# Performance work log

Measured on AMD Instinct MI355X. Metric: run time of the kernel, lower is better.

Reference implementation:

```python
import jax, jax.numpy as jnp
import numpy as np

HEADS = 16
DIM = 1024
D_K = DIM // HEADS
SEQ = 2048


def setup_inputs() -> dict:
    key = jax.random.key(0)
    ks = jax.random.split(key, 11)
    s = 1.0 / np.sqrt(DIM).astype(np.float32)
    return {
        "q": jax.random.normal(ks[0], (SEQ, DIM), jnp.float32),
        "k": jax.random.normal(ks[1], (SEQ, DIM), jnp.float32),
        "v": jax.random.normal(ks[2], (SEQ, DIM), jnp.float32),
        "Wq": jax.random.normal(ks[3], (DIM, DIM), jnp.float32) * s,
        "bq": jax.random.normal(ks[4], (DIM,), jnp.float32) * 0.01,
        "Wk": jax.random.normal(ks[5], (DIM, DIM), jnp.float32) * s,
        "bk": jax.random.normal(ks[6], (DIM,), jnp.float32) * 0.01,
        "Wv": jax.random.normal(ks[7], (DIM, DIM), jnp.float32) * s,
        "bv": jax.random.normal(ks[8], (DIM,), jnp.float32) * 0.01,
        "Wo": jax.random.normal(ks[9], (DIM, DIM), jnp.float32) * s,
        "bo": jax.random.normal(ks[10], (DIM,), jnp.float32) * 0.01,
    }


def reference(q, k, v, Wq, bq, Wk, bk, Wv, bv, Wo, bo):
    S = q.shape[0]
    # torch Linear: x @ W.T + b; view to (1, S, H, d_k) then transpose to (1, H, S, d_k)
    def proj(x, W, b):
        return (x @ W.T + b).reshape(1, S, HEADS, D_K).transpose(0, 2, 1, 3)

    qh = proj(q, Wq, bq)  # (1, H, S, d)
    kh = proj(k, Wk, bk)
    vh = proj(v, Wv, bv)

    scale = 1.0 / np.sqrt(D_K).astype(np.float32)
    scores = jnp.einsum("bhqd,bhkd->bhqk", qh, kh) * scale  # (1, H, S, S)
    # NOTE: source applies softmax over dim=1 == the HEADS axis (faithful quirk)
    attn = jax.nn.softmax(scores, axis=1)
    ctx = jnp.einsum("bhqk,bhkd->bhqd", attn, vh)  # (1, H, S, d)
    concat = ctx.transpose(0, 2, 1, 3).reshape(1, S, DIM)
    return concat @ Wo.T + bo
```

## Files before the change

kernel.cpp:

```cpp
#include <hip/hip_runtime.h>
#include <hip/hip_fp16.h>


typedef _Float16 f16;
typedef _Float16 f16x4 __attribute__((ext_vector_type(4)));
typedef _Float16 f16x8 __attribute__((ext_vector_type(8)));
typedef float    f32x4 __attribute__((ext_vector_type(4)));

#define S_LEN 2048
#define DIM   1024
#define NH    16
#define DK    64
#define EXP2K 0.1803368801111244f

#define MFMA(a, b, c) __builtin_amdgcn_mfma_f32_16x16x32_f16(a, b, c, 0, 0, 0)

#define VM_WAIT0   asm volatile("s_waitcnt vmcnt(0)" ::: "memory")
#define WG_BARRIER asm volatile("s_barrier" ::: "memory")

typedef __attribute__((address_space(1))) void g_void;
typedef __attribute__((address_space(3))) void l_void;

static __device__ __forceinline__ void gload_lds16(const void* g, void* l) {
  __builtin_amdgcn_global_load_lds((g_void*)g, (l_void*)l, 16, 0, 0);
}

static __device__ __forceinline__ float exp_s(float s) {
  return __builtin_amdgcn_exp2f(s * EXP2K);
}

__global__ __launch_bounds__(256) void cvt_all(
    const float* __restrict__ q, const float* __restrict__ k, const float* __restrict__ v,
    const float* __restrict__ Wq, const float* __restrict__ Wk, const float* __restrict__ Wv,
    const float* __restrict__ Wo, f16* __restrict__ qh, f16* __restrict__ kh,
    f16* __restrict__ vh, f16* __restrict__ wqh, f16* __restrict__ wkh,
    f16* __restrict__ wvh, f16* __restrict__ woh) {
  const size_t M = 1048576;
  const int seg = blockIdx.y;
  const float* src;
  f16* dst;
  switch (seg) {
    case 0: src = q;      dst = qh;      break;
    case 1: src = q + M;  dst = qh + M;  break;
    case 2: src = k;      dst = kh;      break;
    case 3: src = k + M;  dst = kh + M;  break;
    case 4: src = v;      dst = vh;      break;
    case 5: src = v + M;  dst = vh + M;  break;
    case 6: src = Wq;     dst = wqh;     break;
    case 7: src = Wk;     dst = wkh;     break;
    case 8: src = Wv;     dst = wvh;     break;
    default: src = Wo;    dst = woh;     break;
  }
  int i = blockIdx.x * 256 + threadIdx.x;
  float4 vv = ((const float4*)src)[i];
  f16x4 o = {(f16)vv.x, (f16)vv.y, (f16)vv.z, (f16)vv.w};
  ((f16x4*)dst)[i] = o;
}

__global__ __launch_bounds__(256) void cvt_f32_f16(const float* __restrict__ src,
                                                   f16* __restrict__ dst, int n4) {
  int i = blockIdx.x * 256 + threadIdx.x;
  if (i < n4) {
    float4 v = ((const float4*)src)[i];
    f16x4 o = {(f16)v.x, (f16)v.y, (f16)v.z, (f16)v.w};
    ((f16x4*)dst)[i] = o;
  }
}

static __device__ __forceinline__ void gemm32_core(const f16* __restrict__ X,
                                                   const f16* __restrict__ W,
                                                   int k0, int k1, int bm, int bn,
                                                   f16* As, f16* Bs,
                                                   f32x4 (&acc)[4][2]) {
  const int tid = threadIdx.x;
  const int wv = tid >> 6;
  const int lane = tid & 63;
  const int qd = lane >> 4;
  const int l16 = lane & 15;
  const int wm = (wv & 1) * 64;
  const int wn = (wv >> 1) * 32;
  const int lr4 = lane >> 2, lc4 = lane & 3;

  const f16* gA = X + (size_t)(bm + wv * 32 + lr4) * DIM + k0 + lc4 * 8;
  const f16* gB = W + (size_t)(bn + wv * 16 + lr4) * DIM + k0 + lc4 * 8;
  const int np = (k1 - k0) >> 5;

  gload_lds16(gA, As + (wv * 32) * 32);
  gload_lds16(gA + 16 * DIM, As + (wv * 32 + 16) * 32);
  gload_lds16(gB, Bs + (wv * 16) * 32);

#pragma unroll 2
  for (int t = 0; t < np; t++) {
    const int buf = t & 1;
    VM_WAIT0;
    WG_BARRIER;
    if (t + 1 < np) {
      const f16* gA1 = gA + (t + 1) * 32;
      const f16* gB1 = gB + (t + 1) * 32;
      f16* dA = As + (buf ^ 1) * (128 * 32);
      f16* dB = Bs + (buf ^ 1) * (64 * 32);
      gload_lds16(gA1, dA + (wv * 32) * 32);
      gload_lds16(gA1 + 16 * DIM, dA + (wv * 32 + 16) * 32);
      gload_lds16(gB1, dB + (wv * 16) * 32);
    }
    const f16* A = As + buf * (128 * 32);
    const f16* B = Bs + buf * (64 * 32);
    f16x8 bf[2];
#pragma unroll
    for (int ni = 0; ni < 2; ni++)
      bf[ni] = *(const f16x8*)&B[(wn + ni * 16 + l16) * 32 + qd * 8];
#pragma unroll
    for (int mi = 0; mi < 4; mi++) {
      f16x8 af = *(const f16x8*)&A[(wm + mi * 16 + l16) * 32 + qd * 8];
#pragma unroll
      for (int ni = 0; ni < 2; ni++)
        acc[mi][ni] = MFMA(af, bf[ni], acc[mi][ni]);
    }
  }
}

__global__ __launch_bounds__(256) void gemm_qkv(
    const f16* __restrict__ X0, const f16* __restrict__ X1, const f16* __restrict__ X2,
    const f16* __restrict__ W0, const f16* __restrict__ W1, const f16* __restrict__ W2,
    const float* __restrict__ b0, const float* __restrict__ b1, const float* __restrict__ b2,
    f16* __restrict__ o0, f16* __restrict__ o1, f16* __restrict__ o2) {
  __shared__ __align__(16) f16 As[2 * 128 * 32];
  __shared__ __align__(16) f16 Bs[2 * 64 * 32];
  const int z = blockIdx.z;
  const f16* X = z == 0 ? X0 : z == 1 ? X1 : X2;
  const f16* W = z == 0 ? W0 : z == 1 ? W1 : W2;
  const float* bias = z == 0 ? b0 : z == 1 ? b1 : b2;
  f16* outh = z == 0 ? o0 : z == 1 ? o1 : o2;

  const int bm = blockIdx.y * 128, bn = blockIdx.x * 64;
  f32x4 acc[4][2];
#pragma unroll
  for (int a = 0; a < 4; a++)
#pragma unroll
    for (int b = 0; b < 2; b++) acc[a][b] = (f32x4){0.f, 0.f, 0.f, 0.f};

  gemm32_core(X, W, 0, DIM, bm, bn, As, Bs, acc);

  const int tid = threadIdx.x;
  const int wv = tid >> 6, lane = tid & 63;
  const int qd = lane >> 4, l16 = lane & 15;
  const int wm = (wv & 1) * 64, wn = (wv >> 1) * 32;
#pragma unroll
  for (int mi = 0; mi < 4; mi++) {
#pragma unroll
    for (int ni = 0; ni < 2; ni++) {
      const int gm = bm + wm + mi * 16 + qd * 4;
      const int gn = bn + wn + ni * 16 + l16;
      const float bs = bias[gn];
      if (z == 2) {
        f16x4 o = {(f16)(acc[mi][ni][0] + bs), (f16)(acc[mi][ni][1] + bs),
                   (f16)(acc[mi][ni][2] + bs), (f16)(acc[mi][ni][3] + bs)};
        *(f16x4*)&outh[(size_t)gn * S_LEN + gm] = o;
      } else {
#pragma unroll
        for (int r = 0; r < 4; r++)
          outh[(size_t)(gm + r) * DIM + gn] = (f16)(acc[mi][ni][r] + bs);
      }
    }
  }
}

__global__ __launch_bounds__(256) void gemm_out(const f16* __restrict__ X,
                                                const f16* __restrict__ W,
                                                const float* __restrict__ bias,
                                                float* __restrict__ outf) {
  __shared__ __align__(16) f16 As[2 * 128 * 32];
  __shared__ __align__(16) f16 Bs[2 * 64 * 32];
  const int z = blockIdx.z;
  const int bm = blockIdx.y * 128, bn = blockIdx.x * 64;
  f32x4 acc[4][2];
#pragma unroll
  for (int a = 0; a < 4; a++)
#pragma unroll
    for (int b = 0; b < 2; b++) acc[a][b] = (f32x4){0.f, 0.f, 0.f, 0.f};

  gemm32_core(X, W, z * (DIM / 2), (z + 1) * (DIM / 2), bm, bn, As, Bs, acc);

  const int tid = threadIdx.x;
  const int wv = tid >> 6, lane = tid & 63;
  const int qd = lane >> 4, l16 = lane & 15;
  const int wm = (wv & 1) * 64, wn = (wv >> 1) * 32;
#pragma unroll
  for (int mi = 0; mi < 4; mi++) {
#pragma unroll
    for (int ni = 0; ni < 2; ni++) {
      const int gm = bm + wm + mi * 16 + qd * 4;
      const int gn = bn + wn + ni * 16 + l16;
      const float bs = z == 0 ? bias[gn] : 0.f;
#pragma unroll
      for (int r = 0; r < 4; r++)
        atomicAdd(&outf[(size_t)(gm + r) * DIM + gn], acc[mi][ni][r] + bs);
    }
  }
}

__global__ __launch_bounds__(256) void attn_denom(const f16* __restrict__ Qp,
                                                  const f16* __restrict__ Kp,
                                                  f16* __restrict__ IDn) {
  __shared__ __align__(16) f16 Qs[2][2][64 * 32];
  __shared__ __align__(16) f16 Ks[2][2][64 * 32];
  const int tid = threadIdx.x;
  const int wv = tid >> 6;
  const int lane = tid & 63;
  const int qd = lane >> 4;
  const int l16 = lane & 15;
  const int wm = (wv & 1) * 32, wn = (wv >> 1) * 32;
  const int bi = blockIdx.y * 64, bj = blockIdx.x * 64;
  const int lr4 = lane >> 2, lc4 = lane & 3;
  const int kkw = wv & 1;
  const int q0 = (wv >> 1) * 2;

  f32x4 dsum[2][2];
#pragma unroll
  for (int a = 0; a < 2; a++)
#pragma unroll
    for (int b = 0; b < 2; b++) dsum[a][b] = (f32x4){0.f, 0.f, 0.f, 0.f};

  {
    const f16* gq = Qp + (size_t)(bi + q0 * 16 + lr4) * DIM + kkw * 32 + lc4 * 8;
    const f16* gk = Kp + (size_t)(bj + q0 * 16 + lr4) * DIM + kkw * 32 + lc4 * 8;
#pragma unroll
    for (int t = 0; t < 2; t++) {
      gload_lds16(gq + (size_t)t * 16 * DIM, &Qs[0][kkw][(q0 + t) * 16 * 32]);
      gload_lds16(gk + (size_t)t * 16 * DIM, &Ks[0][kkw][(q0 + t) * 16 * 32]);
    }
  }

#pragma unroll 2
  for (int h = 0; h < NH; h++) {
    const int buf = h & 1;
    VM_WAIT0;
    WG_BARRIER;
    if (h + 1 < NH) {
      const f16* gq = Qp + (size_t)(bi + q0 * 16 + lr4) * DIM + (h + 1) * DK + kkw * 32 + lc4 * 8;
      const f16* gk = Kp + (size_t)(bj + q0 * 16 + lr4) * DIM + (h + 1) * DK + kkw * 32 + lc4 * 8;
#pragma unroll
      for (int t = 0; t < 2; t++) {
        gload_lds16(gq + (size_t)t * 16 * DIM, &Qs[buf ^ 1][kkw][(q0 + t) * 16 * 32]);
        gload_lds16(gk + (size_t)t * 16 * DIM, &Ks[buf ^ 1][kkw][(q0 + t) * 16 * 32]);
      }
    }

#pragma unroll
    for (int mi = 0; mi < 2; mi++) {
      f16x8 af0 = *(const f16x8*)&Qs[buf][0][(wm + mi * 16 + l16) * 32 + qd * 8];
      f16x8 af1 = *(const f16x8*)&Qs[buf][1][(wm + mi * 16 + l16) * 32 + qd * 8];
#pragma unroll
      for (int ni = 0; ni < 2; ni++) {
        f16x8 bf0 = *(const f16x8*)&Ks[buf][0][(wn + ni * 16 + l16) * 32 + qd * 8];
        f16x8 bf1 = *(const f16x8*)&Ks[buf][1][(wn + ni * 16 + l16) * 32 + qd * 8];
        f32x4 s = {0.f, 0.f, 0.f, 0.f};
        s = MFMA(af0, bf0, s);
        s = MFMA(af1, bf1, s);
#pragma unroll
        for (int r = 0; r < 4; r++) dsum[mi][ni][r] += exp_s(s[r]);
      }
    }
  }
#pragma unroll
  for (int mi = 0; mi < 2; mi++)
#pragma unroll
    for (int ni = 0; ni < 2; ni++)
#pragma unroll
      for (int r = 0; r < 4; r++) {
        const int gi = bi + wm + mi * 16 + qd * 4 + r;
        const int gj = bj + wn + ni * 16 + l16;
        IDn[(size_t)gi * S_LEN + gj] = (f16)(1.f / dsum[mi][ni][r]);
      }
}

__global__ __launch_bounds__(256, 4) void attn_ctx(const f16* __restrict__ Qp,
                                                   const f16* __restrict__ Kp,
                                                   const f16* __restrict__ Vt,
                                                   const f16* __restrict__ IDn,
                                                   float* __restrict__ Cp) {
  __shared__ __align__(16) f16 Ks[2][2][32 * 32];
  __shared__ __align__(16) f16 Vs[2][64 * 32];
  __shared__ __align__(16) f16 Pl[4][32 * 40];
  const int tid = threadIdx.x;
  const int wv = tid >> 6;
  const int lane = tid & 63;
  const int qd = lane >> 4;
  const int l16 = lane & 15;
  const int h = blockIdx.y;
  const int i0 = blockIdx.x * 128;
  const int iw = i0 + wv * 32;
  const int jb = blockIdx.z * 512;
  const int lr4 = lane >> 2, lc4 = lane & 3;
  const int kkw = wv & 1;
  const int rhw = wv >> 1;
  f16* pl = Pl[wv];

  f16x8 aq[2][2];
#pragma unroll
  for (int mi = 0; mi < 2; mi++)
#pragma unroll
    for (int kk = 0; kk < 2; kk++)
      aq[mi][kk] = *(const f16x8*)(Qp + (size_t)(iw + mi * 16 + l16) * DIM +
                                   h * DK + kk * 32 + qd * 8);

  f32x4 acc[2][4];
#pragma unroll
  for (int a = 0; a < 2; a++)
#pragma unroll
    for (int b = 0; b < 4; b++) acc[a][b] = (f32x4){0.f, 0.f, 0.f, 0.f};

  f16x8 idn[2][2];

  {
    const int j0 = jb;
    gload_lds16(Kp + (size_t)(j0 + rhw * 16 + lr4) * DIM + h * DK + kkw * 32 + lc4 * 8,
                &Ks[0][kkw][(rhw * 16) * 32]);
    gload_lds16(Vt + (size_t)(h * DK + wv * 16 + lr4) * S_LEN + j0 + lc4 * 8,
                &Vs[0][(wv * 16) * 32]);
#pragma unroll
    for (int mi = 0; mi < 2; mi++)
      idn[0][mi] = *(const f16x8*)(IDn + (size_t)(iw + mi * 16 + l16) * S_LEN + j0 + qd * 8);
  }

#pragma unroll 2
  for (int jt = 0; jt < 16; jt++) {
    const int buf = jt & 1;
    VM_WAIT0;
    WG_BARRIER;

    if (jt + 1 < 16) {
      const int j1 = jb + (jt + 1) * 32;
      gload_lds16(Kp + (size_t)(j1 + rhw * 16 + lr4) * DIM + h * DK + kkw * 32 + lc4 * 8,
                  &Ks[buf ^ 1][kkw][(rhw * 16) * 32]);
      gload_lds16(Vt + (size_t)(h * DK + wv * 16 + lr4) * S_LEN + j1 + lc4 * 8,
                  &Vs[buf ^ 1][(wv * 16) * 32]);
#pragma unroll
      for (int mi = 0; mi < 2; mi++)
        idn[buf ^ 1][mi] =
            *(const f16x8*)(IDn + (size_t)(iw + mi * 16 + l16) * S_LEN + j1 + qd * 8);
    }

    f16x8 bk[2][2];
#pragma unroll
    for (int ni = 0; ni < 2; ni++)
#pragma unroll
      for (int kk = 0; kk < 2; kk++)
        bk[ni][kk] = *(const f16x8*)&Ks[buf][kk][(ni * 16 + l16) * 32 + qd * 8];
#pragma unroll
    for (int mi = 0; mi < 2; mi++)
#pragma unroll
      for (int ni = 0; ni < 2; ni++) {
        f32x4 s = {0.f, 0.f, 0.f, 0.f};
        s = MFMA(aq[mi][0], bk[ni][0], s);
        s = MFMA(aq[mi][1], bk[ni][1], s);
#pragma unroll
        for (int r = 0; r < 4; r++)
          pl[(mi * 16 + qd * 4 + r) * 40 + ni * 16 + l16] = (f16)exp_s(s[r]);
      }

    f16x8 bv[4];
#pragma unroll
    for (int nd = 0; nd < 4; nd++)
      bv[nd] = *(const f16x8*)&Vs[buf][(nd * 16 + l16) * 32 + qd * 8];
#pragma unroll
    for (int mi = 0; mi < 2; mi++) {
      f16x8 ef = *(const f16x8*)&pl[(mi * 16 + l16) * 40 + qd * 8];
      f16x8 p = ef * idn[buf][mi];
#pragma unroll
      for (int nd = 0; nd < 4; nd++)
        acc[mi][nd] = MFMA(p, bv[nd], acc[mi][nd]);
    }
  }

#pragma unroll
  for (int mi = 0; mi < 2; mi++)
#pragma unroll
    for (int nd = 0; nd < 4; nd++)
#pragma unroll
      for (int r = 0; r < 4; r++)
        atomicAdd(&Cp[(size_t)(iw + mi * 16 + qd * 4 + r) * DIM + h * DK + nd * 16 + l16],
                  acc[mi][nd][r]);
}

extern "C" void kernel_launch(void* const* d_in, const int* in_sizes, int n_in,
                              void* d_out, int out_size, void* d_ws, size_t ws_size,
                              hipStream_t stream) {
  const float* q  = (const float*)d_in[0];
  const float* k  = (const float*)d_in[1];
  const float* v  = (const float*)d_in[2];
  const float* Wq = (const float*)d_in[3];
  const float* bq = (const float*)d_in[4];
  const float* Wk = (const float*)d_in[5];
  const float* bk = (const float*)d_in[6];
  const float* Wv = (const float*)d_in[7];
  const float* bv = (const float*)d_in[8];
  const float* Wo = (const float*)d_in[9];
  const float* bo = (const float*)d_in[10];
  float* out = (float*)d_out;

  f16* w = (f16*)d_ws;
  f16* qh  = w;
  f16* kh  = qh + (size_t)S_LEN * DIM;
  f16* vh  = kh + (size_t)S_LEN * DIM;
  f16* wqh = vh + (size_t)S_LEN * DIM;
  f16* wkh = wqh + (size_t)DIM * DIM;
  f16* wvh = wkh + (size_t)DIM * DIM;
  f16* woh = wvh + (size_t)DIM * DIM;
  f16* Qp  = woh + (size_t)DIM * DIM;
  f16* Kp  = Qp + (size_t)S_LEN * DIM;
  f16* Vt  = Kp + (size_t)S_LEN * DIM;
  f16* IDn = qh;
  float* Cp = (float*)vh;
  f16* Ct  = qh;

  dim3 b256(256);
  cvt_all<<<dim3(1024, 10), b256, 0, stream>>>(q, k, v, Wq, Wk, Wv, Wo,
                                               qh, kh, vh, wqh, wkh, wvh, woh);

  gemm_qkv<<<dim3(DIM / 64, S_LEN / 128, 3), b256, 0, stream>>>(
      qh, kh, vh, wqh, wkh, wvh, bq, bk, bv, Qp, Kp, Vt);

  hipMemsetAsync(Cp, 0, (size_t)S_LEN * DIM * sizeof(float), stream);
  hipMemsetAsync(out, 0, (size_t)S_LEN * DIM * sizeof(float), stream);

  attn_denom<<<dim3(S_LEN / 64, S_LEN / 64), b256, 0, stream>>>(Qp, Kp, IDn);
  attn_ctx<<<dim3(S_LEN / 128, NH, 4), b256, 0, stream>>>(Qp, Kp, Vt, IDn, Cp);

  const int nqkv4 = S_LEN * DIM / 4;
  cvt_f32_f16<<<nqkv4 / 256, b256, 0, stream>>>(Cp, Ct, nqkv4);

  gemm_out<<<dim3(DIM / 64, S_LEN / 128, 2), b256, 0, stream>>>(Ct, woh, bo, out);
}
```

Before: 228.1 us.

## Deepen global-to-LDS prefetch to triple buffering across GEMM and attention kernels

Switches the GEMM core, attn_denom and attn_ctx main loops from double to triple buffering. Each iteration now prefetches two stages ahead and waits on a partial vmcnt instead of draining all outstanding loads, so memory latency overlaps more compute. attn_ctx's loop is manually unrolled by three through a macro so the buffer indices for K, V and the IDn registers stay static. In exchange, LDS use per block grows, which may reduce occupancy, and the vmcnt thresholds must exactly match the number of loads issued per stage.

Measured after the change: 257.6 us. 12.9% more time.

```diff
diff --git a/kernel.cpp b/kernel.cpp
--- a/kernel.cpp
+++ b/kernel.cpp
@@ -16,6 +16,8 @@
 #define MFMA(a, b, c) __builtin_amdgcn_mfma_f32_16x16x32_f16(a, b, c, 0, 0, 0)
 
 #define VM_WAIT0   asm volatile("s_waitcnt vmcnt(0)" ::: "memory")
+#define VM_WAIT3   asm volatile("s_waitcnt vmcnt(3)" ::: "memory")
+#define VM_WAIT4   asm volatile("s_waitcnt vmcnt(4)" ::: "memory")
 #define WG_BARRIER asm volatile("s_barrier" ::: "memory")
 
 typedef __attribute__((address_space(1))) void g_void;
@@ -85,26 +87,26 @@
   const f16* gB = W + (size_t)(bn + wv * 16 + lr4) * DIM + k0 + lc4 * 8;
   const int np = (k1 - k0) >> 5;
 
-  gload_lds16(gA, As + (wv * 32) * 32);
-  gload_lds16(gA + 16 * DIM, As + (wv * 32 + 16) * 32);
-  gload_lds16(gB, Bs + (wv * 16) * 32);
-
-#pragma unroll 2
+#pragma unroll
+  for (int p = 0; p < 2; p++) {
+    gload_lds16(gA + p * 32, As + p * (128 * 32) + (wv * 32) * 32);
+    gload_lds16(gA + p * 32 + 16 * DIM, As + p * (128 * 32) + (wv * 32 + 16) * 32);
+    gload_lds16(gB + p * 32, Bs + p * (64 * 32) + (wv * 16) * 32);
+  }
+
+  int b0 = 0;
   for (int t = 0; t < np; t++) {
-    const int buf = t & 1;
-    VM_WAIT0;
+    if (t == np - 1) { VM_WAIT0; } else { VM_WAIT3; }
     WG_BARRIER;
-    if (t + 1 < np) {
-      const f16* gA1 = gA + (t + 1) * 32;
-      const f16* gB1 = gB + (t + 1) * 32;
-      f16* dA = As + (buf ^ 1) * (128 * 32);
-      f16* dB = Bs + (buf ^ 1) * (64 * 32);
-      gload_lds16(gA1, dA + (wv * 32) * 32);
-      gload_lds16(gA1 + 16 * DIM, dA + (wv * 32 + 16) * 32);
-      gload_lds16(gB1, dB + (wv * 16) * 32);
-    }
-    const f16* A = As + buf * (128 * 32);
-    const f16* B = Bs + buf * (64 * 32);
+    if (t + 2 < np) {
+      int b2 = b0 + 2; if (b2 >= 3) b2 -= 3;
+      const f16* gA2 = gA + (t + 2) * 32;
+      gload_lds16(gA2, As + b2 * (128 * 32) + (wv * 32) * 32);
+      gload_lds16(gA2 + 16 * DIM, As + b2 * (128 * 32) + (wv * 32 + 16) * 32);
+      gload_lds16(gB + (t + 2) * 32, Bs + b2 * (64 * 32) + (wv * 16) * 32);
+    }
+    const f16* A = As + b0 * (128 * 32);
+    const f16* B = Bs + b0 * (64 * 32);
     f16x8 bf[2];
 #pragma unroll
     for (int ni = 0; ni < 2; ni++)
@@ -116,6 +118,7 @@
       for (int ni = 0; ni < 2; ni++)
         acc[mi][ni] = MFMA(af, bf[ni], acc[mi][ni]);
     }
+    b0 = (b0 == 2) ? 0 : b0 + 1;
   }
 }
 
@@ -124,8 +127,8 @@
     const f16* __restrict__ W0, const f16* __restrict__ W1, const f16* __restrict__ W2,
     const float* __restrict__ b0, const float* __restrict__ b1, const float* __restrict__ b2,
     f16* __restrict__ o0, f16* __restrict__ o1, f16* __restrict__ o2) {
-  __shared__ __align__(16) f16 As[2 * 128 * 32];
-  __shared__ __align__(16) f16 Bs[2 * 64 * 32];
+  __shared__ __align__(16) f16 As[3 * 128 * 32];
+  __shared__ __align__(16) f16 Bs[3 * 64 * 32];
   const int z = blockIdx.z;
   const f16* X = z == 0 ? X0 : z == 1 ? X1 : X2;
   const f16* W = z == 0 ? W0 : z == 1 ? W1 : W2;
@@ -169,8 +172,8 @@
                                                 const f16* __restrict__ W,
                                                 const float* __restrict__ bias,
                                                 float* __restrict__ outf) {
-  __shared__ __align__(16) f16 As[2 * 128 * 32];
-  __shared__ __align__(16) f16 Bs[2 * 64 * 32];
+  __shared__ __align__(16) f16 As[3 * 128 * 32];
+  __shared__ __align__(16) f16 Bs[3 * 64 * 32];
   const int z = blockIdx.z;
   const int bm = blockIdx.y * 128, bn = blockIdx.x * 64;
   f32x4 acc[4][2];
@@ -202,8 +205,8 @@
 __global__ __launch_bounds__(256) void attn_denom(const f16* __restrict__ Qp,
                                                   const f16* __restrict__ Kp,
                                                   f16* __restrict__ IDn) {
-  __shared__ __align__(16) f16 Qs[2][2][64 * 32];
-  __shared__ __align__(16) f16 Ks[2][2][64 * 32];
+  __shared__ __align__(16) f16 Qs[3][2][64 * 32];
+  __shared__ __align__(16) f16 Ks[3][2][64 * 32];
   const int tid = threadIdx.x;
   const int wv = tid >> 6;
   const int lane = tid & 63;
@@ -221,39 +224,41 @@
 #pragma unroll
     for (int b = 0; b < 2; b++) dsum[a][b] = (f32x4){0.f, 0.f, 0.f, 0.f};
 
-  {
-    const f16* gq = Qp + (size_t)(bi + q0 * 16 + lr4) * DIM + kkw * 32 + lc4 * 8;
-    const f16* gk = Kp + (size_t)(bj + q0 * 16 + lr4) * DIM + kkw * 32 + lc4 * 8;
+#pragma unroll
+  for (int p = 0; p < 2; p++) {
+    const f16* gq = Qp + (size_t)(bi + q0 * 16 + lr4) * DIM + p * DK + kkw * 32 + lc4 * 8;
+    const f16* gk = Kp + (size_t)(bj + q0 * 16 + lr4) * DIM + p * DK + kkw * 32 + lc4 * 8;
 #pragma unroll
     for (int t = 0; t < 2; t++) {
-      gload_lds16(gq + (size_t)t * 16 * DIM, &Qs[0][kkw][(q0 + t) * 16 * 32]);
-      gload_lds16(gk + (size_t)t * 16 * DIM, &Ks[0][kkw][(q0 + t) * 16 * 32]);
-    }
-  }
-
-#pragma unroll 2
+      gload_lds16(gq + (size_t)t * 16 * DIM, &Qs[p][kkw][(q0 + t) * 16 * 32]);
+      gload_lds16(gk + (size_t)t * 16 * DIM, &Ks[p][kkw][(q0 + t) * 16 * 32]);
+    }
+  }
+
+  int b0 = 0;
   for (int h = 0; h < NH; h++) {
-    const int buf = h & 1;
-    VM_WAIT0;
+    if (h == NH - 1) { VM_WAIT0; } else { VM_WAIT4; }
     WG_BARRIER;
-    if (h + 1 < NH) {
-      const f16* gq = Qp + (size_t)(bi + q0 * 16 + lr4) * DIM + (h + 1) * DK + kkw * 32 + lc4 * 8;
-      const f16* gk = Kp + (size_t)(bj + q0 * 16 + lr4) * DIM + (h + 1) * DK + kkw * 32 + lc4 * 8;
+    if (h + 2 < NH) {
+      int b2 = b0 + 2; if (b2 >= 3) b2 -= 3;
+      const int hc = (h + 2) * DK;
+      const f16* gq = Qp + (size_t)(bi + q0 * 16 + lr4) * DIM + hc + kkw * 32 + lc4 * 8;
+      const f16* gk = Kp + (size_t)(bj + q0 * 16 + lr4) * DIM + hc + kkw * 32 + lc4 * 8;
 #pragma unroll
       for (int t = 0; t < 2; t++) {
-        gload_lds16(gq + (size_t)t * 16 * DIM, &Qs[buf ^ 1][kkw][(q0 + t) * 16 * 32]);
-        gload_lds16(gk + (size_t)t * 16 * DIM, &Ks[buf ^ 1][kkw][(q0 + t) * 16 * 32]);
+        gload_lds16(gq + (size_t)t * 16 * DIM, &Qs[b2][kkw][(q0 + t) * 16 * 32]);
+        gload_lds16(gk + (size_t)t * 16 * DIM, &Ks[b2][kkw][(q0 + t) * 16 * 32]);
       }
     }
 
 #pragma unroll
     for (int mi = 0; mi < 2; mi++) {
-      f16x8 af0 = *(const f16x8*)&Qs[buf][0][(wm + mi * 16 + l16) * 32 + qd * 8];
-      f16x8 af1 = *(const f16x8*)&Qs[buf][1][(wm + mi * 16 + l16) * 32 + qd * 8];
+      f16x8 af0 = *(const f16x8*)&Qs[b0][0][(wm + mi * 16 + l16) * 32 + qd * 8];
+      f16x8 af1 = *(const f16x8*)&Qs[b0][1][(wm + mi * 16 + l16) * 32 + qd * 8];
 #pragma unroll
       for (int ni = 0; ni < 2; ni++) {
-        f16x8 bf0 = *(const f16x8*)&Ks[buf][0][(wn + ni * 16 + l16) * 32 + qd * 8];
-        f16x8 bf1 = *(const f16x8*)&Ks[buf][1][(wn + ni * 16 + l16) * 32 + qd * 8];
+        f16x8 bf0 = *(const f16x8*)&Ks[b0][0][(wn + ni * 16 + l16) * 32 + qd * 8];
+        f16x8 bf1 = *(const f16x8*)&Ks[b0][1][(wn + ni * 16 + l16) * 32 + qd * 8];
         f32x4 s = {0.f, 0.f, 0.f, 0.f};
         s = MFMA(af0, bf0, s);
         s = MFMA(af1, bf1, s);
@@ -261,6 +266,7 @@
         for (int r = 0; r < 4; r++) dsum[mi][ni][r] += exp_s(s[r]);
       }
     }
+    b0 = (b0 == 2) ? 0 : b0 + 1;
   }
 #pragma unroll
   for (int mi = 0; mi < 2; mi++)
@@ -274,13 +280,57 @@
       }
 }
 
+#define CTX_PERIOD(T, B, NB)                                                              \
+  {                                                                                       \
+    if ((T) == 15) { VM_WAIT0; } else { VM_WAIT4; }                                       \
+    WG_BARRIER;                                                                           \
+    if ((T) + 2 < 16) {                                                                   \
+      const int j2 = jb + ((T) + 2) * 32;                                                 \
+      gload_lds16(Kp + (size_t)(j2 + rhw * 16 + lr4) * DIM + h * DK + kkw * 32 + lc4 * 8, \
+                  &Ks[NB][kkw][(rhw * 16) * 32]);                                         \
+      gload_lds16(Vt + (size_t)(h * DK + wv * 16 + lr4) * S_LEN + j2 + lc4 * 8,           \
+                  &Vs[NB][(wv * 16) * 32]);                                               \
+      idn[NB][0] = *(const f16x8*)(IDn + (size_t)(iw + l16) * S_LEN + j2 + qd * 8);       \
+      idn[NB][1] = *(const f16x8*)(IDn + (size_t)(iw + 16 + l16) * S_LEN + j2 + qd * 8);  \
+    }                                                                                     \
+    f16x8 bk[2][2];                                                                       \
+    _Pragma("unroll")                                                                     \
+    for (int ni = 0; ni < 2; ni++)                                                        \
+      _Pragma("unroll")                                                                   \
+      for (int kk = 0; kk < 2; kk++)                                                      \
+        bk[ni][kk] = *(const f16x8*)&Ks[B][kk][(ni * 16 + l16) * 32 + qd * 8];            \
+    _Pragma("unroll")                                                                     \
+    for (int mi = 0; mi < 2; mi++)                                                        \
+      _Pragma("unroll")                                                                   \
+      for (int ni = 0; ni < 2; ni++) {                                                    \
+        f32x4 s = {0.f, 0.f, 0.f, 0.f};                                                   \
+        s = MFMA(aq[mi][0], bk[ni][0], s);                                                \
+        s = MFMA(aq[mi][1], bk[ni][1], s);                                                \
+        _Pragma("unroll")                                                                 \
+        for (int r = 0; r < 4; r++)                                                       \
+          pl[(mi * 16 + qd * 4 + r) * 40 + ni * 16 + l16] = (f16)exp_s(s[r]);             \
+      }                                                                                   \
+    f16x8 bv[4];                                                                          \
+    _Pragma("unroll")                                                                     \
+    for (int nd = 0; nd < 4; nd++)                                                        \
+      bv[nd] = *(const f16x8*)&Vs[B][(nd * 16 + l16) * 32 + qd * 8];                      \
+    _Pragma("unroll")                                                                     \
+    for (int mi = 0; mi < 2; mi++) {                                                      \
+      f16x8 ef = *(const f16x8*)&pl[(mi * 16 + l16) * 40 + qd * 8];                       \
+      f16x8 p = ef * idn[B][mi];                                                          \
+      _Pragma("unroll")                                                                   \
+      for (int nd = 0; nd < 4; nd++)                                                      \
+        acc[mi][nd] = MFMA(p, bv[nd], acc[mi][nd]);                                       \
+    }                                                                                     \
+  }
+
 __global__ __launch_bounds__(256, 4) void attn_ctx(const f16* __restrict__ Qp,
                                                    const f16* __restrict__ Kp,
                                                    const f16* __restrict__ Vt,
                                                    const f16* __restrict__ IDn,
                                                    float* __restrict__ Cp) {
-  __shared__ __align__(16) f16 Ks[2][2][32 * 32];
-  __shared__ __align__(16) f16 Vs[2][64 * 32];
+  __shared__ __align__(16) f16 Ks[3][2][32 * 32];
+  __shared__ __align__(16) f16 Vs[3][64 * 32];
   __shared__ __align__(16) f16 Pl[4][32 * 40];
   const int tid = threadIdx.x;
   const int wv = tid >> 6;
@@ -310,68 +360,25 @@
 #pragma unroll
     for (int b = 0; b < 4; b++) acc[a][b] = (f32x4){0.f, 0.f, 0.f, 0.f};
 
-  f16x8 idn[2][2];
-
-  {
-    const int j0 = jb;
+  f16x8 idn[3][2];
+
+#pragma unroll
+  for (int p = 0; p < 2; p++) {
+    const int j0 = jb + p * 32;
     gload_lds16(Kp + (size_t)(j0 + rhw * 16 + lr4) * DIM + h * DK + kkw * 32 + lc4 * 8,
-                &Ks[0][kkw][(rhw * 16) * 32]);
+                &Ks[p][kkw][(rhw * 16) * 32]);
     gload_lds16(Vt + (size_t)(h * DK + wv * 16 + lr4) * S_LEN + j0 + lc4 * 8,
-                &Vs[0][(wv * 16) * 32]);
-#pragma unroll
-    for (int mi = 0; mi < 2; mi++)
-      idn[0][mi] = *(const f16x8*)(IDn + (size_t)(iw + mi * 16 + l16) * S_LEN + j0 + qd * 8);
-  }
-
-#pragma unroll 2
-  for (int jt = 0; jt < 16; jt++) {
-    const int buf = jt & 1;
-    VM_WAIT0;
-    WG_BARRIER;
-
-    if (jt + 1 < 16) {
-      const int j1 = jb + (jt + 1) * 32;
-      gload_lds16(Kp + (size_t)(j1 + rhw * 16 + lr4) * DIM + h * DK + kkw * 32 + lc4 * 8,
-                  &Ks[buf ^ 1][kkw][(rhw * 16) * 32]);
-      gload_lds16(Vt + (size_t)(h * DK + wv * 16 + lr4) * S_LEN + j1 + lc4 * 8,
-                  &Vs[buf ^ 1][(wv * 16) * 32]);
-#pragma unroll
-      for (int mi = 0; mi < 2; mi++)
-        idn[buf ^ 1][mi] =
-            *(const f16x8*)(IDn + (size_t)(iw + mi * 16 + l16) * S_LEN + j1 + qd * 8);
-    }
-
-    f16x8 bk[2][2];
-#pragma unroll
-    for (int ni = 0; ni < 2; ni++)
-#pragma unroll
-      for (int kk = 0; kk < 2; kk++)
-        bk[ni][kk] = *(const f16x8*)&Ks[buf][kk][(ni * 16 + l16) * 32 + qd * 8];
-#pragma unroll
-    for (int mi = 0; mi < 2; mi++)
-#pragma unroll
-      for (int ni = 0; ni < 2; ni++) {
-        f32x4 s = {0.f, 0.f, 0.f, 0.f};
-        s = MFMA(aq[mi][0], bk[ni][0], s);
-        s = MFMA(aq[mi][1], bk[ni][1], s);
-#pragma unroll
-        for (int r = 0; r < 4; r++)
-          pl[(mi * 16 + qd * 4 + r) * 40 + ni * 16 + l16] = (f16)exp_s(s[r]);
-      }
-
-    f16x8 bv[4];
-#pragma unroll
-    for (int nd = 0; nd < 4; nd++)
-      bv[nd] = *(const f16x8*)&Vs[buf][(nd * 16 + l16) * 32 + qd * 8];
-#pragma unroll
-    for (int mi = 0; mi < 2; mi++) {
-      f16x8 ef = *(const f16x8*)&pl[(mi * 16 + l16) * 40 + qd * 8];
-      f16x8 p = ef * idn[buf][mi];
-#pragma unroll
-      for (int nd = 0; nd < 4; nd++)
-        acc[mi][nd] = MFMA(p, bv[nd], acc[mi][nd]);
-    }
-  }
+                &Vs[p][(wv * 16) * 32]);
+    idn[p][0] = *(const f16x8*)(IDn + (size_t)(iw + l16) * S_LEN + j0 + qd * 8);
+    idn[p][1] = *(const f16x8*)(IDn + (size_t)(iw + 16 + l16) * S_LEN + j0 + qd * 8);
+  }
+
+  for (int tt = 0; tt < 15; tt += 3) {
+    CTX_PERIOD(tt, 0, 2);
+    CTX_PERIOD(tt + 1, 1, 0);
+    CTX_PERIOD(tt + 2, 2, 1);
+  }
+  CTX_PERIOD(15, 0, 0);
 
 #pragma unroll
   for (int mi = 0; mi < 2; mi++)
```

## Keep P in registers via transposed score MFMA and fold output zeroing into convert kernel

Applied to the files above, without the earlier changes.

The attention context kernel now computes scores transposed (K as A operand, Q as B), so each lane's accumulator rows line up with the 16x16x16 MFMA A-operand layout. The exp-weighted probabilities can then be fed straight into the PV product without the per-wave LDS round trip, and the per-key normalisation loads are reshaped to f16x4 to match. Separately, zeroing of the output buffer moves from a memset into two extra grid rows of the conversion kernel, removing one launch. The trade-off is that the PV product now uses the smaller 16x16x16 MFMA, so twice as many MFMA instructions are issued.

Result: slower. 236.2 us (+3.5%).

```diff
diff --git a/kernel.cpp b/kernel.cpp
--- a/kernel.cpp
+++ b/kernel.cpp
@@ -13,7 +13,8 @@
 #define DK    64
 #define EXP2K 0.1803368801111244f
 
-#define MFMA(a, b, c) __builtin_amdgcn_mfma_f32_16x16x32_f16(a, b, c, 0, 0, 0)
+#define MFMA(a, b, c)   __builtin_amdgcn_mfma_f32_16x16x32_f16(a, b, c, 0, 0, 0)
+#define MFMA16(a, b, c) __builtin_amdgcn_mfma_f32_16x16x16f16(a, b, c, 0, 0, 0)
 
 #define VM_WAIT0   asm volatile("s_waitcnt vmcnt(0)" ::: "memory")
 #define WG_BARRIER asm volatile("s_barrier" ::: "memory")
@@ -34,9 +35,15 @@
     const float* __restrict__ Wq, const float* __restrict__ Wk, const float* __restrict__ Wv,
     const float* __restrict__ Wo, f16* __restrict__ qh, f16* __restrict__ kh,
     f16* __restrict__ vh, f16* __restrict__ wqh, f16* __restrict__ wkh,
-    f16* __restrict__ wvh, f16* __restrict__ woh) {
+    f16* __restrict__ wvh, f16* __restrict__ woh, float* __restrict__ outz) {
   const size_t M = 1048576;
   const int seg = blockIdx.y;
+  int i = blockIdx.x * 256 + threadIdx.x;
+  if (seg >= 10) {
+    float4 z4 = {0.f, 0.f, 0.f, 0.f};
+    ((float4*)(outz + (size_t)(seg - 10) * M))[i] = z4;
+    return;
+  }
   const float* src;
   f16* dst;
   switch (seg) {
@@ -51,7 +58,6 @@
     case 8: src = Wv;     dst = wvh;     break;
     default: src = Wo;    dst = woh;     break;
   }
-  int i = blockIdx.x * 256 + threadIdx.x;
   float4 vv = ((const float4*)src)[i];
   f16x4 o = {(f16)vv.x, (f16)vv.y, (f16)vv.z, (f16)vv.w};
   ((f16x4*)dst)[i] = o;
@@ -281,7 +287,6 @@
                                                    float* __restrict__ Cp) {
   __shared__ __align__(16) f16 Ks[2][2][32 * 32];
   __shared__ __align__(16) f16 Vs[2][64 * 32];
-  __shared__ __align__(16) f16 Pl[4][32 * 40];
   const int tid = threadIdx.x;
   const int wv = tid >> 6;
   const int lane = tid & 63;
@@ -294,7 +299,6 @@
   const int lr4 = lane >> 2, lc4 = lane & 3;
   const int kkw = wv & 1;
   const int rhw = wv >> 1;
-  f16* pl = Pl[wv];
 
   f16x8 aq[2][2];
 #pragma unroll
@@ -310,7 +314,7 @@
 #pragma unroll
     for (int b = 0; b < 4; b++) acc[a][b] = (f32x4){0.f, 0.f, 0.f, 0.f};
 
-  f16x8 idn[2][2];
+  f16x4 idn[2][2][2];
 
   {
     const int j0 = jb;
@@ -320,7 +324,10 @@
                 &Vs[0][(wv * 16) * 32]);
 #pragma unroll
     for (int mi = 0; mi < 2; mi++)
-      idn[0][mi] = *(const f16x8*)(IDn + (size_t)(iw + mi * 16 + l16) * S_LEN + j0 + qd * 8);
+#pragma unroll
+      for (int ni = 0; ni < 2; ni++)
+        idn[0][mi][ni] = *(const f16x4*)(IDn + (size_t)(iw + mi * 16 + l16) * S_LEN +
+                                         j0 + ni * 16 + qd * 4);
   }
 
 #pragma unroll 2
@@ -337,8 +344,10 @@
                   &Vs[buf ^ 1][(wv * 16) * 32]);
 #pragma unroll
       for (int mi = 0; mi < 2; mi++)
-        idn[buf ^ 1][mi] =
-            *(const f16x8*)(IDn + (size_t)(iw + mi * 16 + l16) * S_LEN + j1 + qd * 8);
+#pragma unroll
+        for (int ni = 0; ni < 2; ni++)
+          idn[buf ^ 1][mi][ni] = *(const f16x4*)(IDn + (size_t)(iw + mi * 16 + l16) * S_LEN +
+                                                 j1 + ni * 16 + qd * 4);
     }
 
     f16x8 bk[2][2];
@@ -347,29 +356,26 @@
 #pragma unroll
       for (int kk = 0; kk < 2; kk++)
         bk[ni][kk] = *(const f16x8*)&Ks[buf][kk][(ni * 16 + l16) * 32 + qd * 8];
-#pragma unroll
-    for (int mi = 0; mi < 2; mi++)
-#pragma unroll
-      for (int ni = 0; ni < 2; ni++) {
-        f32x4 s = {0.f, 0.f, 0.f, 0.f};
-        s = MFMA(aq[mi][0], bk[ni][0], s);
-        s = MFMA(aq[mi][1], bk[ni][1], s);
+
+#pragma unroll
+    for (int ni = 0; ni < 2; ni++) {
+      f16x4 bv[4];
+#pragma unroll
+      for (int nd = 0; nd < 4; nd++)
+        bv[nd] = *(const f16x4*)&Vs[buf][(nd * 16 + l16) * 32 + ni * 16 + qd * 4];
+#pragma unroll
+      for (int mi = 0; mi < 2; mi++) {
+        f32x4 st = {0.f, 0.f, 0.f, 0.f};
+        st = MFMA(bk[ni][0], aq[mi][0], st);
+        st = MFMA(bk[ni][1], aq[mi][1], st);
+        f16x4 p;
 #pragma unroll
         for (int r = 0; r < 4; r++)
-          pl[(mi * 16 + qd * 4 + r) * 40 + ni * 16 + l16] = (f16)exp_s(s[r]);
+          p[r] = (f16)(exp_s(st[r]) * (float)idn[buf][mi][ni][r]);
+#pragma unroll
+        for (int nd = 0; nd < 4; nd++)
+          acc[mi][nd] = MFMA16(p, bv[nd], acc[mi][nd]);
       }
-
-    f16x8 bv[4];
-#pragma unroll
-    for (int nd = 0; nd < 4; nd++)
-      bv[nd] = *(const f16x8*)&Vs[buf][(nd * 16 + l16) * 32 + qd * 8];
-#pragma unroll
-    for (int mi = 0; mi < 2; mi++) {
-      f16x8 ef = *(const f16x8*)&pl[(mi * 16 + l16) * 40 + qd * 8];
-      f16x8 p = ef * idn[buf][mi];
-#pragma unroll
-      for (int nd = 0; nd < 4; nd++)
-        acc[mi][nd] = MFMA(p, bv[nd], acc[mi][nd]);
     }
   }
 
@@ -415,14 +421,13 @@
   f16* Ct  = qh;
 
   dim3 b256(256);
-  cvt_all<<<dim3(1024, 10), b256, 0, stream>>>(q, k, v, Wq, Wk, Wv, Wo,
-                                               qh, kh, vh, wqh, wkh, wvh, woh);
+  cvt_all<<<dim3(1024, 12), b256, 0, stream>>>(q, k, v, Wq, Wk, Wv, Wo,
+                                               qh, kh, vh, wqh, wkh, wvh, woh, out);
 
   gemm_qkv<<<dim3(DIM / 64, S_LEN / 128, 3), b256, 0, stream>>>(
       qh, kh, vh, wqh, wkh, wvh, bq, bk, bv, Qp, Kp, Vt);
 
   hipMemsetAsync(Cp, 0, (size_t)S_LEN * DIM * sizeof(float), stream);
-  hipMemsetAsync(out, 0, (size_t)S_LEN * DIM * sizeof(float), stream);
 
   attn_denom<<<dim3(S_LEN / 64, S_LEN / 64), b256, 0, stream>>>(Qp, Kp, IDn);
   attn_ctx<<<dim3(S_LEN / 128, NH, 4), b256, 0, stream>>>(Qp, Kp, Vt, IDn, Cp);
```
